# Optimization experiments

Hardware: AMD Instinct MI355X
Metric: run time of the kernel (lower is better)

## Reference

```python
import jax, jax.numpy as jnp
import numpy as np

HIDDEN = 1024
HEADS = 16
HEAD_DIM = HIDDEN // HEADS


def setup_inputs() -> dict:
    key = jax.random.key(0)
    ks = jax.random.split(key, 7)
    B, S = 2, 2048
    scale = 1.0 / np.sqrt(HIDDEN)
    return {
        "hidden_states": jax.random.normal(ks[0], (B, S, HIDDEN), dtype=jnp.float32),
        "attention_mask": jnp.zeros((B, S), dtype=jnp.float32),
        "Wq": jax.random.normal(ks[1], (HIDDEN, HIDDEN), dtype=jnp.float32) * scale,
        "bq": jnp.zeros((HIDDEN,), dtype=jnp.float32),
        "Wk": jax.random.normal(ks[2], (HIDDEN, HIDDEN), dtype=jnp.float32) * scale,
        "bk": jnp.zeros((HIDDEN,), dtype=jnp.float32),
        "Wv": jax.random.normal(ks[3], (HIDDEN, HIDDEN), dtype=jnp.float32) * scale,
        "bv": jnp.zeros((HIDDEN,), dtype=jnp.float32),
    }


def reference(hidden_states, attention_mask, Wq, bq, Wk, bk, Wv, bv):
    B, S, _ = hidden_states.shape
    def heads(x):  # [B,S,HIDDEN] -> [B,H,S,D]
        return x.reshape(B, S, HEADS, HEAD_DIM).transpose(0, 2, 1, 3)
    q = heads(hidden_states @ Wq + bq)
    k = heads(hidden_states @ Wk + bk)
    v = heads(hidden_states @ Wv + bv)
    scores = jnp.einsum('bhqd,bhkd->bhqk', q, k) / np.sqrt(HEAD_DIM).astype(np.float32)
    # additive mask broadcast [B,1,1,S]
    scores = scores + attention_mask[:, None, None, :]
    probs = jax.nn.softmax(scores, axis=-1)
    # dropout is identity in eval mode (reference baseline)
    ctx = jnp.einsum('bhqk,bhkd->bhqd', probs, v)
    return ctx.transpose(0, 2, 1, 3).reshape(B, S, HIDDEN)
```

## Files before the change

kernel.cpp:

```cpp
#include <hip/hip_runtime.h>
#include <cstdint>
#include <cstddef>

typedef __bf16 bf16;
typedef __attribute__((ext_vector_type(8))) __bf16 bf16x8;
typedef __attribute__((ext_vector_type(4))) float f32x4;
typedef __attribute__((ext_vector_type(16))) float f32x16;

#define MFMA16(a, b, c) __builtin_amdgcn_mfma_f32_16x16x32_bf16((a), (b), (c), 0, 0, 0)
#define MFMA32(a, b, c) __builtin_amdgcn_mfma_f32_32x32x16_bf16((a), (b), (c), 0, 0, 0)

static constexpr int BB   = 2;
static constexpr int SS   = 2048;
static constexpr int HID  = 1024;
static constexpr int NH   = 16;
static constexpr int HD   = 64;
static constexpr int MROW = BB * SS;
static constexpr int NQKV = 3 * HID;
static constexpr float LOG2E = 1.4426950408889634f;
static constexpr float MSHIFT = 16.0f;

__device__ __forceinline__ int SW(int r) { return ((r ^ (r >> 3)) & 7) << 4; }

__device__ __forceinline__ uint32_t pack_bf16(float a, float b) {
    union { bf16 h[2]; uint32_t u; } x;
    x.h[0] = (bf16)a; x.h[1] = (bf16)b;
    return x.u;
}

__device__ __forceinline__ uint32_t pack_raw(bf16 a, bf16 b) {
    union { bf16 h[2]; uint32_t u; } x;
    x.h[0] = a; x.h[1] = b;
    return x.u;
}

__device__ __forceinline__ float exp2i(float x) {
    float r; asm("v_exp_f32 %0, %1" : "=v"(r) : "v"(x)); return r;
}

__device__ __forceinline__ void plswap(uint32_t& a, uint32_t& b) {
    asm("v_permlane32_swap_b32 %0, %1" : "+v"(a), "+v"(b));
}

__device__ __forceinline__ void gload16(const void* g, void* l) {
    __builtin_amdgcn_global_load_lds(
        (const __attribute__((address_space(1))) void*)g,
        (__attribute__((address_space(3))) void*)l, 16, 0, 0);
}

__global__ __launch_bounds__(256) void cvt_hidden(const float* __restrict__ in,
                                                  bf16* __restrict__ out) {
    const int i = (blockIdx.x * 256 + threadIdx.x) * 8;
    float4 f0 = *(const float4*)&in[i];
    float4 f1 = *(const float4*)&in[i + 4];
    bf16x8 o;
    o[0] = (bf16)f0.x; o[1] = (bf16)f0.y; o[2] = (bf16)f0.z; o[3] = (bf16)f0.w;
    o[4] = (bf16)f1.x; o[5] = (bf16)f1.y; o[6] = (bf16)f1.z; o[7] = (bf16)f1.w;
    *(bf16x8*)&out[i] = o;
}

__global__ __launch_bounds__(256) void maskcvt(const float* __restrict__ m,
                                               float* __restrict__ o) {
    const int i = blockIdx.x * 256 + threadIdx.x;
    o[i] = m[i] * LOG2E - MSHIFT;
}

__global__ __launch_bounds__(256) void wtrans(const float* __restrict__ Wq,
                                              const float* __restrict__ Wk,
                                              const float* __restrict__ Wv,
                                              bf16* __restrict__ Wt) {
    __shared__ float tile[32][33];
    const float* W = (blockIdx.z == 0) ? Wq : (blockIdx.z == 1) ? Wk : Wv;
    bf16* O = Wt + (size_t)blockIdx.z * HID * HID;
    const int x  = blockIdx.x * 32 + threadIdx.x;
    const int y0 = blockIdx.y * 32;
#pragma unroll
    for (int i = threadIdx.y; i < 32; i += 8)
        tile[i][threadIdx.x] = W[(size_t)(y0 + i) * HID + x];
    __syncthreads();
    const int k = y0 + threadIdx.x;
#pragma unroll
    for (int i = threadIdx.y; i < 32; i += 8)
        O[(size_t)(blockIdx.x * 32 + i) * HID + k] = (bf16)tile[threadIdx.x][i];
}

__global__ __launch_bounds__(256) void qkv_gemm(
    const bf16* __restrict__ A, const bf16* __restrict__ Bt,
    const float* __restrict__ bq, const float* __restrict__ bk,
    const float* __restrict__ bv,
    bf16* __restrict__ Qo, bf16* __restrict__ Ko, bf16* __restrict__ Vo) {
    __shared__ __align__(16) bf16 As[128 * 32];
    __shared__ __align__(16) bf16 Bs[128 * 32];
    const int t = threadIdx.x, l = t & 63;
    const int l15 = l & 15, l4 = l >> 4;
    const int w = t >> 6;
    const int wm = w >> 1, wn = w & 1;
    const int m0 = blockIdx.y * 128, n0 = blockIdx.x * 128;

    f32x4 acc[4][4] = {};

    for (int kt = 0; kt < 32; ++kt) {
        const int k0 = kt * 32;
        __syncthreads();
#pragma unroll
        for (int cc = 0; cc < 2; ++cc) {
            const int c = t + cc * 256;
            const int row = c >> 2, col = (c & 3) * 8;
            gload16(&A[(size_t)(m0 + row) * HID + k0 + col], (char*)As + c * 16);
            gload16(&Bt[(size_t)(n0 + row) * HID + k0 + col], (char*)Bs + c * 16);
        }
        __syncthreads();

        bf16x8 af[4], bf_[4];
#pragma unroll
        for (int mi = 0; mi < 4; ++mi) {
            const int r = wm * 64 + mi * 16 + l15;
            af[mi] = *(const bf16x8*)((const char*)As + r * 64 + l4 * 16);
        }
#pragma unroll
        for (int ni = 0; ni < 4; ++ni) {
            const int r = wn * 64 + ni * 16 + l15;
            bf_[ni] = *(const bf16x8*)((const char*)Bs + r * 64 + l4 * 16);
        }
        __builtin_amdgcn_s_setprio(1);
#pragma unroll
        for (int mi = 0; mi < 4; ++mi)
#pragma unroll
            for (int ni = 0; ni < 4; ++ni)
                acc[mi][ni] = MFMA16(af[mi], bf_[ni], acc[mi][ni]);
        __builtin_amdgcn_s_setprio(0);
    }

#pragma unroll
    for (int mi = 0; mi < 4; ++mi) {
#pragma unroll
        for (int ni = 0; ni < 4; ++ni) {
            const int ng = n0 + wn * 64 + ni * 16 + l15;
            const int qkv = ng >> 10;
            const int nn = ng & 1023;
            const int hh = nn >> 6, dd = nn & 63;
            const float* bp = (qkv == 0) ? bq : (qkv == 1) ? bk : bv;
            bf16* op = (qkv == 0) ? Qo : (qkv == 1) ? Ko : Vo;
            const float bias = bp[nn];
            const float scl = (qkv == 0) ? 0.125f * LOG2E : 1.0f;
            const int mg = m0 + wm * 64 + mi * 16 + l4 * 4;
            const int bb = mg >> 11, ss = mg & 2047;
            bf16* dst = op + ((size_t)(bb * NH + hh) * SS + ss) * HD + dd;
#pragma unroll
            for (int j = 0; j < 4; ++j)
                dst[(size_t)j * HD] = (bf16)((acc[mi][ni][j] + bias) * scl);
        }
    }
}

__global__ __launch_bounds__(256) void attn_fwd(
    const bf16* __restrict__ Q, const bf16* __restrict__ K,
    const bf16* __restrict__ V, const float* __restrict__ mkl,
    float* __restrict__ Op, float* __restrict__ ml) {
    __shared__ __align__(16) char Ks0[64 * 128];
    __shared__ __align__(16) char Ks1[64 * 128];
    __shared__ __align__(16) char Vt0[64 * 128];
    __shared__ __align__(16) char Vt1[64 * 128];

    const int t = threadIdx.x, l = t & 63, w = t >> 6;
    const int l31 = l & 31, h = l >> 5;

    const int bid = blockIdx.x;
    const int nid = (bid & 7) * 128 + (bid >> 3);
    const int bh = nid >> 5, kh = (nid >> 4) & 1, qb = nid & 15;
    const int q0 = qb * 128 + w * 32;
    const int kbase = kh * (SS / 2);

    const bf16* Qp = Q + (size_t)bh * SS * HD;
    const bf16* Kp = K + (size_t)bh * SS * HD;
    const bf16* Vp = V + (size_t)bh * SS * HD;
    const float* mkp = mkl + (bh >> 4) * SS;

    bf16x8 qf[4];
#pragma unroll
    for (int c = 0; c < 4; ++c)
        qf[c] = *(const bf16x8*)&Qp[(size_t)(q0 + l31) * HD + c * 16 + h * 8];

    float lrun = 0.f;
    f32x16 o0 = {}, o1 = {};

    const int vp_ = t >> 3, vdb = (t & 7) * 8;

    auto stageK = [&](int tile, char* dst) {
        const int key0 = kbase + tile * 64;
#pragma unroll
        for (int cc = 0; cc < 2; ++cc) {
            const int c = t + cc * 256;
            const int row = c >> 3;
            const int csw = (c & 7) ^ ((row ^ (row >> 3)) & 7);
            gload16(&Kp[(size_t)(key0 + row) * HD + csw * 8], dst + c * 16);
        }
    };
    auto loadV = [&](int tile, bf16x8& va, bf16x8& vb) {
        const int key0 = kbase + tile * 64;
        va = *(const bf16x8*)&Vp[(size_t)(key0 + 2 * vp_) * HD + vdb];
        vb = *(const bf16x8*)&Vp[(size_t)(key0 + 2 * vp_ + 1) * HD + vdb];
    };
    auto storeV = [&](char* Vtn, const bf16x8& va, const bf16x8& vb) {
#pragma unroll
        for (int i = 0; i < 8; ++i) {
            const int d = vdb + i;
            *(uint32_t*)(Vtn + d * 128 + ((vp_ * 4) ^ SW(d))) =
                pack_raw(va[i], vb[i]);
        }
    };

    stageK(0, Ks0);
    {
        bf16x8 va, vb;
        loadV(0, va, vb);
        storeV(Vt0, va, vb);
    }
    __syncthreads();

    constexpr int NT = (SS / 2) / 64;
#pragma unroll 1
    for (int kt = 0; kt < NT; ++kt) {
        char* Ks = (kt & 1) ? Ks1 : Ks0;
        char* Vt = (kt & 1) ? Vt1 : Vt0;
        char* Ksn = (kt & 1) ? Ks0 : Ks1;
        char* Vtn = (kt & 1) ? Vt0 : Vt1;
        const int key0 = kbase + kt * 64;
        const bool more = (kt + 1) < NT;

        bf16x8 va = {}, vb = {};
        if (more) {
            stageK(kt + 1, Ksn);
            loadV(kt + 1, va, vb);
        }

        f32x16 s0, s1;
#pragma unroll
        for (int rq = 0; rq < 4; ++rq) {
            const f32x4 m0v = *(const f32x4*)&mkp[key0 + rq * 8 + 4 * h];
            const f32x4 m1v = *(const f32x4*)&mkp[key0 + 32 + rq * 8 + 4 * h];
#pragma unroll
            for (int j = 0; j < 4; ++j) {
                s0[rq * 4 + j] = m0v[j];
                s1[rq * 4 + j] = m1v[j];
            }
        }
        __builtin_amdgcn_s_setprio(1);
#pragma unroll
        for (int c = 0; c < 4; ++c) {
            const int r0 = l31;
            bf16x8 kf0 = *(const bf16x8*)(Ks + r0 * 128 +
                                          ((c * 32 + h * 16) ^ SW(r0)));
            s0 = MFMA32(kf0, qf[c], s0);
        }
#pragma unroll
        for (int c = 0; c < 4; ++c) {
            const int r1 = 32 + l31;
            bf16x8 kf1 = *(const bf16x8*)(Ks + r1 * 128 +
                                          ((c * 32 + h * 16) ^ SW(r1)));
            s1 = MFMA32(kf1, qf[c], s1);
        }
        __builtin_amdgcn_s_setprio(0);

#pragma unroll
        for (int g = 0; g < 2; ++g) {
            f32x16& st = g ? s1 : s0;
            float ps = 0.f;
#pragma unroll
            for (int r = 0; r < 16; ++r) {
                const float p = exp2i(st[r]);
                st[r] = p;
                ps += p;
            }
            lrun += ps;
#pragma unroll
            for (int cc = 0; cc < 2; ++cc) {
                uint32_t wA = pack_bf16(st[8 * cc + 0], st[8 * cc + 1]);
                uint32_t wB = pack_bf16(st[8 * cc + 2], st[8 * cc + 3]);
                uint32_t wC = pack_bf16(st[8 * cc + 4], st[8 * cc + 5]);
                uint32_t wD = pack_bf16(st[8 * cc + 6], st[8 * cc + 7]);
                plswap(wA, wC);
                plswap(wB, wD);
                union { uint32_t u[4]; bf16x8 v; } pb;
                pb.u[0] = wA; pb.u[1] = wB; pb.u[2] = wC; pb.u[3] = wD;
                const int colb = g * 64 + cc * 32 + h * 16;
                __builtin_amdgcn_s_setprio(1);
                {
                    bf16x8 vf0 = *(const bf16x8*)(Vt + l31 * 128 +
                                                  (colb ^ SW(l31)));
                    o0 = MFMA32(vf0, pb.v, o0);
                    const int r1 = 32 + l31;
                    bf16x8 vf1 = *(const bf16x8*)(Vt + r1 * 128 +
                                                  (colb ^ SW(r1)));
                    o1 = MFMA32(vf1, pb.v, o1);
                }
                __builtin_amdgcn_s_setprio(0);
            }
            if (g == 0 && more) storeV(Vtn, va, vb);
        }
        __syncthreads();
    }

    lrun += __shfl_xor(lrun, 32);
    const int part = kh * 512 + bh * 16 + qb;
    float* Ob = Op + (size_t)part * 8192;
    const int row = w * 32 + l31;
#pragma unroll
    for (int rq = 0; rq < 4; ++rq) {
        f32x4 a, b2;
#pragma unroll
        for (int j = 0; j < 4; ++j) { a[j] = o0[rq * 4 + j]; b2[j] = o1[rq * 4 + j]; }
        *(f32x4*)&Ob[row * 64 + rq * 8 + 4 * h] = a;
        *(f32x4*)&Ob[row * 64 + 32 + rq * 8 + 4 * h] = b2;
    }
    if (l < 32) ml[(size_t)part * 128 + (w * 32 + l)] = lrun;
}

__global__ __launch_bounds__(256) void combine(
    const float* __restrict__ Op, const float* __restrict__ ml,
    float* __restrict__ out) {
    const int tid = blockIdx.x * 256 + threadIdx.x;
    const int dg = tid & 15, gq = tid >> 4;
    const int bh = gq >> 11, s = gq & 2047;
    const int qb = s >> 7, q = s & 127;
    const int p0 = bh * 16 + qb, p1 = 512 + p0;

    const float l1 = ml[(size_t)p0 * 128 + q];
    const float l2 = ml[(size_t)p1 * 128 + q];
    const float inv = 1.0f / (l1 + l2);

    const f32x4 O1 = *(const f32x4*)&Op[(size_t)p0 * 8192 + q * 64 + dg * 4];
    const f32x4 O2 = *(const f32x4*)&Op[(size_t)p1 * 8192 + q * 64 + dg * 4];
    f32x4 r;
#pragma unroll
    for (int i = 0; i < 4; ++i) r[i] = (O1[i] + O2[i]) * inv;

    const int b = bh >> 4, hh = bh & 15;
    *(f32x4*)&out[((size_t)(b * SS + s)) * HID + hh * HD + dg * 4] = r;
}

extern "C" void kernel_launch(void* const* d_in, const int* in_sizes, int n_in,
                              void* d_out, int out_size, void* d_ws, size_t ws_size,
                              hipStream_t stream) {
    (void)in_sizes; (void)n_in; (void)out_size; (void)ws_size;
    const float* hs  = (const float*)d_in[0];
    const float* msk = (const float*)d_in[1];
    const float* Wq  = (const float*)d_in[2];
    const float* bq  = (const float*)d_in[3];
    const float* Wk  = (const float*)d_in[4];
    const float* bk  = (const float*)d_in[5];
    const float* Wv  = (const float*)d_in[6];
    const float* bv  = (const float*)d_in[7];
    float* out = (float*)d_out;
    char* ws = (char*)d_ws;
    const size_t MB = 1 << 20;

    bf16* Qb  = (bf16*)ws;
    bf16* Kb  = (bf16*)(ws + 8 * MB);
    bf16* Vb  = (bf16*)(ws + 16 * MB);
    float* mk2 = (float*)(ws + 24 * MB);
    bf16* Xb  = (bf16*)(ws + 25 * MB);
    bf16* Wt  = (bf16*)(ws + 33 * MB);
    float* Opp = (float*)(ws + 25 * MB);
    float* mlp = (float*)(ws + 59 * MB);

    cvt_hidden<<<dim3(MROW * HID / (256 * 8)), dim3(256), 0, stream>>>(hs, Xb);
    maskcvt<<<dim3(BB * SS / 256), dim3(256), 0, stream>>>(msk, mk2);
    wtrans<<<dim3(32, 32, 3), dim3(32, 8), 0, stream>>>(Wq, Wk, Wv, Wt);
    qkv_gemm<<<dim3(NQKV / 128, MROW / 128), dim3(256), 0, stream>>>(
        Xb, Wt, bq, bk, bv, Qb, Kb, Vb);
    attn_fwd<<<dim3(1024), dim3(256), 0, stream>>>(Qb, Kb, Vb, mk2, Opp, mlp);
    combine<<<dim3(4096), dim3(256), 0, stream>>>(Opp, mlp, out);
}
```

Baseline: 122.6 us.

## Compute softmax row sums via MFMA with ones and store partials in fp16

Drops the per-element VALU accumulation of softmax denominators and computes them instead with an extra MFMA that multiplies a ones matrix by the packed probabilities. The partial output accumulators are written as fp16 instead of fp32, which halves partial-buffer traffic. The combine kernel reads 8 halves per thread and launches half as many blocks. In exchange this adds one MFMA per PV step, sums bf16-rounded probabilities rather than fp32 ones, and risks fp16 range or precision loss on the unnormalized partials.

Result: faster. 120.1 us (-2.1%).

```diff
diff --git a/kernel.cpp b/kernel.cpp
--- a/kernel.cpp
+++ b/kernel.cpp
@@ -3,9 +3,12 @@
 #include <cstddef>
 
 typedef __bf16 bf16;
+typedef _Float16 f16;
 typedef __attribute__((ext_vector_type(8))) __bf16 bf16x8;
 typedef __attribute__((ext_vector_type(4))) float f32x4;
 typedef __attribute__((ext_vector_type(16))) float f32x16;
+typedef __attribute__((ext_vector_type(4))) _Float16 f16x4;
+typedef __attribute__((ext_vector_type(8))) _Float16 f16x8;
 
 #define MFMA16(a, b, c) __builtin_amdgcn_mfma_f32_16x16x32_bf16((a), (b), (c), 0, 0, 0)
 #define MFMA32(a, b, c) __builtin_amdgcn_mfma_f32_32x32x16_bf16((a), (b), (c), 0, 0, 0)
@@ -156,7 +159,7 @@
 __global__ __launch_bounds__(256) void attn_fwd(
     const bf16* __restrict__ Q, const bf16* __restrict__ K,
     const bf16* __restrict__ V, const float* __restrict__ mkl,
-    float* __restrict__ Op, float* __restrict__ ml) {
+    f16* __restrict__ Op, float* __restrict__ ml) {
     __shared__ __align__(16) char Ks0[64 * 128];
     __shared__ __align__(16) char Ks1[64 * 128];
     __shared__ __align__(16) char Vt0[64 * 128];
@@ -181,8 +184,12 @@
     for (int c = 0; c < 4; ++c)
         qf[c] = *(const bf16x8*)&Qp[(size_t)(q0 + l31) * HD + c * 16 + h * 8];
 
-    float lrun = 0.f;
+    bf16x8 ones;
+#pragma unroll
+    for (int i = 0; i < 8; ++i) ones[i] = (bf16)1.0f;
+
     f32x16 o0 = {}, o1 = {};
+    f32x16 o2 = {};
 
     const int vp_ = t >> 3, vdb = (t & 7) * 8;
 
@@ -265,14 +272,8 @@
 #pragma unroll
         for (int g = 0; g < 2; ++g) {
             f32x16& st = g ? s1 : s0;
-            float ps = 0.f;
-#pragma unroll
-            for (int r = 0; r < 16; ++r) {
-                const float p = exp2i(st[r]);
-                st[r] = p;
-                ps += p;
-            }
-            lrun += ps;
+#pragma unroll
+            for (int r = 0; r < 16; ++r) st[r] = exp2i(st[r]);
 #pragma unroll
             for (int cc = 0; cc < 2; ++cc) {
                 uint32_t wA = pack_bf16(st[8 * cc + 0], st[8 * cc + 1]);
@@ -286,6 +287,7 @@
                 const int colb = g * 64 + cc * 32 + h * 16;
                 __builtin_amdgcn_s_setprio(1);
                 {
+                    o2 = MFMA32(ones, pb.v, o2);
                     bf16x8 vf0 = *(const bf16x8*)(Vt + l31 * 128 +
                                                   (colb ^ SW(l31)));
                     o0 = MFMA32(vf0, pb.v, o0);
@@ -301,26 +303,28 @@
         __syncthreads();
     }
 
-    lrun += __shfl_xor(lrun, 32);
     const int part = kh * 512 + bh * 16 + qb;
-    float* Ob = Op + (size_t)part * 8192;
+    f16* Ob = Op + (size_t)part * 8192;
     const int row = w * 32 + l31;
 #pragma unroll
     for (int rq = 0; rq < 4; ++rq) {
-        f32x4 a, b2;
-#pragma unroll
-        for (int j = 0; j < 4; ++j) { a[j] = o0[rq * 4 + j]; b2[j] = o1[rq * 4 + j]; }
-        *(f32x4*)&Ob[row * 64 + rq * 8 + 4 * h] = a;
-        *(f32x4*)&Ob[row * 64 + 32 + rq * 8 + 4 * h] = b2;
-    }
-    if (l < 32) ml[(size_t)part * 128 + (w * 32 + l)] = lrun;
+        f16x4 a, b2;
+#pragma unroll
+        for (int j = 0; j < 4; ++j) {
+            a[j]  = (f16)o0[rq * 4 + j];
+            b2[j] = (f16)o1[rq * 4 + j];
+        }
+        *(f16x4*)&Ob[row * 64 + rq * 8 + 4 * h] = a;
+        *(f16x4*)&Ob[row * 64 + 32 + rq * 8 + 4 * h] = b2;
+    }
+    if (l < 32) ml[(size_t)part * 128 + (w * 32 + l)] = o2[0];
 }
 
 __global__ __launch_bounds__(256) void combine(
-    const float* __restrict__ Op, const float* __restrict__ ml,
+    const f16* __restrict__ Op, const float* __restrict__ ml,
     float* __restrict__ out) {
     const int tid = blockIdx.x * 256 + threadIdx.x;
-    const int dg = tid & 15, gq = tid >> 4;
+    const int dg = tid & 7, gq = tid >> 3;
     const int bh = gq >> 11, s = gq & 2047;
     const int qb = s >> 7, q = s & 127;
     const int p0 = bh * 16 + qb, p1 = 512 + p0;
@@ -329,14 +333,19 @@
     const float l2 = ml[(size_t)p1 * 128 + q];
     const float inv = 1.0f / (l1 + l2);
 
-    const f32x4 O1 = *(const f32x4*)&Op[(size_t)p0 * 8192 + q * 64 + dg * 4];
-    const f32x4 O2 = *(const f32x4*)&Op[(size_t)p1 * 8192 + q * 64 + dg * 4];
-    f32x4 r;
-#pragma unroll
-    for (int i = 0; i < 4; ++i) r[i] = (O1[i] + O2[i]) * inv;
+    const f16x8 O1 = *(const f16x8*)&Op[(size_t)p0 * 8192 + q * 64 + dg * 8];
+    const f16x8 O2 = *(const f16x8*)&Op[(size_t)p1 * 8192 + q * 64 + dg * 8];
+    f32x4 r0, r1;
+#pragma unroll
+    for (int i = 0; i < 4; ++i) {
+        r0[i] = ((float)O1[i] + (float)O2[i]) * inv;
+        r1[i] = ((float)O1[4 + i] + (float)O2[4 + i]) * inv;
+    }
 
     const int b = bh >> 4, hh = bh & 15;
-    *(f32x4*)&out[((size_t)(b * SS + s)) * HID + hh * HD + dg * 4] = r;
+    float* op = &out[((size_t)(b * SS + s)) * HID + hh * HD + dg * 8];
+    *(f32x4*)op = r0;
+    *(f32x4*)(op + 4) = r1;
 }
 
 extern "C" void kernel_launch(void* const* d_in, const int* in_sizes, int n_in,
@@ -361,7 +370,7 @@
     float* mk2 = (float*)(ws + 24 * MB);
     bf16* Xb  = (bf16*)(ws + 25 * MB);
     bf16* Wt  = (bf16*)(ws + 33 * MB);
-    float* Opp = (float*)(ws + 25 * MB);
+    f16* Opp  = (f16*)(ws + 25 * MB);
     float* mlp = (float*)(ws + 59 * MB);
 
     cvt_hidden<<<dim3(MROW * HID / (256 * 8)), dim3(256), 0, stream>>>(hs, Xb);
@@ -370,5 +379,5 @@
     qkv_gemm<<<dim3(NQKV / 128, MROW / 128), dim3(256), 0, stream>>>(
         Xb, Wt, bq, bk, bv, Qb, Kb, Vb);
     attn_fwd<<<dim3(1024), dim3(256), 0, stream>>>(Qb, Kb, Vb, mk2, Opp, mlp);
-    combine<<<dim3(4096), dim3(256), 0, stream>>>(Opp, mlp, out);
-}
+    combine<<<dim3(2048), dim3(256), 0, stream>>>(Opp, mlp, out);
+}
```
